# Performance work log

Measured on AMD Instinct MI355X. Metric: run time of the kernel, lower is better.

The kernel has to match this reference:

```python
import jax, jax.numpy as jnp
import numpy as np

N = 50000      # nodes
E = 800000     # edges
D = 128        # input feature dim
H = 8          # heads
U = 32         # units per head (model width = H*U = 256)
L = 2          # attention layers
OUT = 64       # output dim


def setup_inputs() -> dict:
    key = jax.random.key(0)
    ks = jax.random.split(key, 8)
    node_states = jax.random.normal(ks[0], (N, D), jnp.float32)
    edges = jax.random.randint(ks[1], (E, 2), 0, N, jnp.int32)
    s = 0.05  # small init scale keeps pre-clip scores in a sane range
    W_pre = jax.random.normal(ks[2], (D, H * U), jnp.float32) * s
    b_pre = jnp.zeros((H * U,), jnp.float32)
    W_att = jax.random.normal(ks[3], (L, H, H * U, U), jnp.float32) * s
    a_att = jax.random.normal(ks[4], (L, H, 2 * U), jnp.float32) * s
    W_out = jax.random.normal(ks[5], (H * U, OUT), jnp.float32) * s
    b_out = jnp.zeros((OUT,), jnp.float32)
    return {"node_states": node_states, "edges": edges, "W_pre": W_pre,
            "b_pre": b_pre, "W_att": W_att, "a_att": a_att,
            "W_out": W_out, "b_out": b_out}


def _gat_multihead(x, src, dst, W, a):
    """One MultiHeadGraphAttention layer. x:[N,HU], W:[H,HU,U], a:[H,2U].
    Returns relu(concat over heads):[N,HU]."""
    n = x.shape[0]
    h = jnp.einsum('nd,hdu->hnu', x, W)                     # [H,N,U]
    # concat([h_src, h_dst]) @ a  ==  a_src.h_src + a_dst.h_dst
    s_src = jnp.einsum('hnu,hu->hn', h, a[:, :U])           # [H,N]
    s_dst = jnp.einsum('hnu,hu->hn', h, a[:, U:])           # [H,N]
    e = jax.nn.leaky_relu(s_src[:, src] + s_dst[:, dst], negative_slope=0.2)
    e = jnp.exp(jnp.clip(e, -2.0, 2.0))                     # [H,E]
    den = jax.vmap(lambda v: jax.ops.segment_sum(v, src, num_segments=n))(e)
    alpha = e / den[:, src]                                 # [H,E]
    msgs = h[:, dst, :] * alpha[..., None]                  # [H,E,U]
    agg = jax.vmap(lambda m: jax.ops.segment_sum(m, src, num_segments=n))(msgs)
    return jax.nn.relu(agg.transpose(1, 0, 2).reshape(n, -1))  # [N,HU]


def reference(node_states, edges, W_pre, b_pre, W_att, a_att, W_out, b_out):
    src, dst = edges[:, 0], edges[:, 1]
    x = jax.nn.relu(node_states @ W_pre + b_pre)            # [N,HU]
    for l in range(L):
        x = _gat_multihead(x, src, dst, W_att[l], a_att[l]) + x
    return x @ W_out + b_out                                # [N,OUT]
```

## Files before the change

### kernel.cpp

```cpp
#include <hip/hip_runtime.h>
#include <hip/hip_bf16.h>
#include <hip/hip_fp8.h>

#define N_NODES 50000
#define E_EDGES 800000
#define D_IN    128
#define HU      256
#define H_HEADS 8
#define U_DIM   32
#define OUT_DIM 64
#define CAP     64
#define H_SCALE 32.0f

typedef __attribute__((ext_vector_type(8))) short short8v;
typedef __attribute__((ext_vector_type(4))) float f32x4;
typedef unsigned short u16;
typedef unsigned char u8;
typedef __attribute__((ext_vector_type(4))) unsigned short u16x4;
typedef __attribute__((ext_vector_type(8))) unsigned short u16x8;

__device__ __forceinline__ float bf2f(u16 v) {
    return __uint_as_float(((unsigned)v) << 16);
}
__device__ __forceinline__ u16 f2b(float f) {
    unsigned u = __float_as_uint(f);
    return (u16)((u + 0x7FFFu + ((u >> 16) & 1u)) >> 16);
}
__device__ __forceinline__ u8 f2fp8(float f) {
    __hip_fp8_e4m3 t(f);
    return (u8)t.__x;
}

__global__ __launch_bounds__(256) void adj_fill(const int* __restrict__ edges,
                                                int* __restrict__ deg,
                                                u16* __restrict__ adj) {
    int tid = blockIdx.x * 256 + threadIdx.x;
    if (tid >= E_EDGES / 4) return;
    const int4* E4 = (const int4*)edges;
    int4 p0 = E4[tid * 2];
    int4 p1 = E4[tid * 2 + 1];
    int sx[4] = {p0.x, p0.z, p1.x, p1.z};
    int dx[4] = {p0.y, p0.w, p1.y, p1.w};
    int slot[4];
#pragma unroll
    for (int i = 0; i < 4; ++i)
        slot[i] = atomicAdd(&deg[sx[i]], 1);
#pragma unroll
    for (int i = 0; i < 4; ++i)
        if (slot[i] < CAP) adj[(size_t)sx[i] * CAP + slot[i]] = (u16)dx[i];
}

template<int K, int N, bool GAT>
__device__ __forceinline__ void wfrag_one(const float* __restrict__ W,
                                          u16* __restrict__ Wf, int tid) {
    int j  = tid & 7;
    int l  = (tid >> 3) & 63;
    int fb = tid >> 9;
    int ks = fb % (K / 32);
    int ct = fb / (K / 32);
    int k  = ks * 32 + (l >> 4) * 8 + j;
    int n  = ct * 16 + (l & 15);
    float v = GAT ? W[(size_t)(n >> 5) * (K * 32) + k * 32 + (n & 31)]
                  : W[(size_t)k * N + n];
    Wf[tid] = f2b(v);
}

__device__ __forceinline__ void wa_one(const float* __restrict__ Watt,
                                       const float* __restrict__ al,
                                       u16* __restrict__ Wfs, int tid) {
    int j  = tid & 7;
    int l  = (tid >> 3) & 63;
    int ks = tid >> 9;
    int k  = ks * 32 + (l >> 4) * 8 + j;
    int n  = l & 15;
    int hd = n & 7;
    int off = (n < 8) ? 0 : 32;
    float s = 0.f;
#pragma unroll
    for (int u = 0; u < 32; ++u)
        s += Watt[(size_t)hd * 8192 + k * 32 + u] * al[hd * 64 + off + u];
    Wfs[tid] = f2b(s);
}

__global__ __launch_bounds__(256) void wfrag_all(const float* __restrict__ Wpre,
                                                 const float* __restrict__ Watt,
                                                 const float* __restrict__ aatt,
                                                 const float* __restrict__ Wout,
                                                 u16* __restrict__ wf_pre,
                                                 u16* __restrict__ wf_a0,
                                                 u16* __restrict__ wf_a1,
                                                 u16* __restrict__ wf_out,
                                                 u16* __restrict__ wfs0,
                                                 u16* __restrict__ wfs1) {
    int tid = blockIdx.x * 256 + threadIdx.x;
    if (tid < 32768)        wfrag_one<D_IN, HU, false>(Wpre, wf_pre, tid);
    else if (tid < 98304)   wfrag_one<HU, HU, true>(Watt, wf_a0, tid - 32768);
    else if (tid < 163840)  wfrag_one<HU, HU, true>(Watt + 65536, wf_a1, tid - 98304);
    else if (tid < 180224)  wfrag_one<HU, OUT_DIM, false>(Wout, wf_out, tid - 163840);
    else if (tid < 184320)  wa_one(Watt, aatt, wfs0, tid - 180224);
    else if (tid < 188416)  wa_one(Watt + 65536, aatt + 512, wfs1, tid - 184320);
}

template<int K, int N, int MT, int NT, int MODE, bool ABF16>
__global__ __launch_bounds__(256) void mfma_gemm(const void* __restrict__ Ain,
                                                 const u16* __restrict__ Wf,
                                                 const float* __restrict__ bias,
                                                 void* __restrict__ Cout,
                                                 const u16* __restrict__ wfs,
                                                 u16* __restrict__ sb,
                                                 u16* __restrict__ db) {
    constexpr int SK = K + 8;
    __shared__ __align__(16) u16 as[64 * SK];
    int t  = threadIdx.x;
    int n0 = blockIdx.x * 64;

    if (ABF16) {
        constexpr int K8 = K / 8;
        const u16x8* A8 = (const u16x8*)Ain;
        for (int i = t; i < 64 * K8; i += 256) {
            int row = i / K8, c8 = i % K8;
            u16x8 v = {0, 0, 0, 0, 0, 0, 0, 0};
            if (n0 + row < N_NODES)
                v = __builtin_nontemporal_load(&A8[(size_t)(n0 + row) * K8 + c8]);
            *(u16x8*)&as[row * SK + c8 * 8] = v;
        }
    } else {
        constexpr int K4 = K / 4;
        const f32x4* A4 = (const f32x4*)Ain;
        for (int i = t; i < 64 * K4; i += 256) {
            int row = i / K4, c4 = i % K4;
            f32x4 v = {0.f, 0.f, 0.f, 0.f};
            if (n0 + row < N_NODES)
                v = __builtin_nontemporal_load(&A4[(size_t)(n0 + row) * K4 + c4]);
            u16x4 pk;
            pk.x = f2b(v.x); pk.y = f2b(v.y); pk.z = f2b(v.z); pk.w = f2b(v.w);
            *(u16x4*)&as[row * SK + c4 * 4] = pk;
        }
    }
    __syncthreads();

    int wid = t >> 6, l = t & 63;
    constexpr int NWN = N / (NT * 16);
    int col0 = (wid % NWN) * (NT * 16);
    int row0 = (wid / NWN) * (MT * 16);

    f32x4 acc[MT][NT];
#pragma unroll
    for (int mt = 0; mt < MT; ++mt)
#pragma unroll
        for (int nt = 0; nt < NT; ++nt)
            acc[mt][nt] = (f32x4){0.f, 0.f, 0.f, 0.f};
    f32x4 accs[MT];
#pragma unroll
    for (int mt = 0; mt < MT; ++mt) accs[mt] = (f32x4){0.f, 0.f, 0.f, 0.f};

    int ar  = l & 15;
    int akb = (l >> 4) * 8;
#pragma unroll
    for (int ks = 0; ks < K / 32; ++ks) {
        short8v a[MT], b[NT];
#pragma unroll
        for (int mt = 0; mt < MT; ++mt)
            a[mt] = *(const short8v*)&as[(row0 + mt * 16 + ar) * SK + ks * 32 + akb];
#pragma unroll
        for (int nt = 0; nt < NT; ++nt)
            b[nt] = *(const short8v*)&Wf[(size_t)(((((col0 >> 4) + nt) * (K / 32)) + ks) * 64 + l) * 8];
        if (MODE == 1) {
            if (wid == 0) {
                short8v bs = *(const short8v*)&wfs[(size_t)(ks * 64 + l) * 8];
#pragma unroll
                for (int mt = 0; mt < MT; ++mt)
                    accs[mt] = __builtin_amdgcn_mfma_f32_16x16x32_bf16(a[mt], bs, accs[mt], 0, 0, 0);
            }
        }
#pragma unroll
        for (int mt = 0; mt < MT; ++mt)
#pragma unroll
            for (int nt = 0; nt < NT; ++nt)
                acc[mt][nt] = __builtin_amdgcn_mfma_f32_16x16x32_bf16(a[mt], b[nt], acc[mt][nt], 0, 0, 0);
    }

    int crow = (l >> 4) * 4, ccol = l & 15;
#pragma unroll
    for (int mt = 0; mt < MT; ++mt) {
#pragma unroll
        for (int nt = 0; nt < NT; ++nt) {
            int gc = col0 + nt * 16 + ccol;
#pragma unroll
            for (int r = 0; r < 4; ++r) {
                int gr = n0 + row0 + mt * 16 + crow + r;
                if (gr >= N_NODES) continue;
                float v = acc[mt][nt][r];
                if (MODE == 0) {
                    v += bias[gc];
                    ((u16*)Cout)[(size_t)gr * N + gc] = f2b(fmaxf(v, 0.f));
                } else if (MODE == 1) {
                    ((u8*)Cout)[(size_t)gr * N + gc] = f2fp8(v * H_SCALE);
                } else {
                    ((float*)Cout)[(size_t)gr * N + gc] = v + bias[gc];
                }
            }
        }
    }
    if (MODE == 1) {
        if (wid == 0) {
#pragma unroll
            for (int mt = 0; mt < MT; ++mt) {
#pragma unroll
                for (int r = 0; r < 4; ++r) {
                    int gr = n0 + mt * 16 + crow + r;
                    if (gr >= N_NODES) continue;
                    float v = accs[mt][r];
                    if (ccol < 8) sb[(size_t)gr * 8 + ccol] = f2b(v);
                    else          db[(size_t)gr * 8 + ccol - 8] = f2b(v);
                }
            }
        }
    }
}

__global__ __launch_bounds__(256) void agg_kernel(const u8* __restrict__ hb,
                                                  const u16* __restrict__ ssrcb,
                                                  const u16* __restrict__ sdstb,
                                                  const int* __restrict__ deg,
                                                  const u16* __restrict__ adj,
                                                  u16* __restrict__ x) {
    __shared__ u16 sd_lds[4][64 * 8];
    int t  = threadIdx.x & 63;
    int wv = threadIdx.x >> 6;
    int n  = blockIdx.x * 4 + wv;
    int dg = deg[n];
    dg = dg > CAP ? CAP : dg;
    int dl = (t < dg) ? (int)__builtin_nontemporal_load(&adj[(size_t)n * CAP + t]) : 0;
    u16x8 sdrow = *(const u16x8*)(sdstb + (size_t)dl * 8);
    *(u16x8*)&sd_lds[wv][t * 8] = sdrow;
    __syncthreads();

    int hd8 = t & 7;
    float ss_s = bf2f(ssrcb[(size_t)n * 8 + hd8]);
    int q   = t >> 4;
    int sub = t & 15;
    int hdg = sub >> 1;

    float a[16];
#pragma unroll
    for (int i = 0; i < 16; ++i) a[i] = 0.f;
    float den_part = 0.f;

    for (int base = 0; base < dg; base += 8) {
        int eidx = base + (t >> 3);
        float w = 0.f;
        if (eidx < dg) {
            float sc = ss_s + bf2f(sd_lds[wv][eidx * 8 + hd8]);
            sc = sc > 0.f ? sc : 0.2f * sc;
            sc = fminf(fmaxf(sc, -2.f), 2.f);
            w = __expf(sc);
        }
        den_part += w;
#pragma unroll
        for (int g = 0; g < 2; ++g) {
            int e4 = base + g * 4 + q;
            int d  = __shfl(dl, e4);
            float we = __shfl(w, ((g * 4 + q) << 3) | hdg);
            if (e4 < dg) {
                uint4 hv = *(const uint4*)(hb + (size_t)d * HU + sub * 16);
#pragma unroll
                for (int i = 0; i < 4; ++i) {
                    unsigned dw = (&hv.x)[i];
                    auto lo = __builtin_amdgcn_cvt_pk_f32_fp8(dw, false);
                    auto hi = __builtin_amdgcn_cvt_pk_f32_fp8(dw, true);
                    a[4 * i + 0] += we * lo[0];
                    a[4 * i + 1] += we * lo[1];
                    a[4 * i + 2] += we * hi[0];
                    a[4 * i + 3] += we * hi[1];
                }
            }
        }
    }

    den_part += __shfl_xor(den_part, 8);
    den_part += __shfl_xor(den_part, 16);
    den_part += __shfl_xor(den_part, 32);
#pragma unroll
    for (int i = 0; i < 16; ++i) {
        a[i] += __shfl_xor(a[i], 16);
        a[i] += __shfl_xor(a[i], 32);
    }

    if (q == 0) {
        float den = __shfl(den_part, hdg);
        float inv = dg > 0 ? (1.f / den) * (1.f / H_SCALE) : 0.f;
        size_t xo = (size_t)n * HU + sub * 16;
        u16x8 xv0 = __builtin_nontemporal_load((const u16x8*)(x + xo));
        u16x8 xv1 = __builtin_nontemporal_load((const u16x8*)(x + xo + 8));
        u16x8 o0, o1;
#pragma unroll
        for (int i = 0; i < 8; ++i) {
            o0[i] = f2b(fmaxf(a[i] * inv, 0.f) + bf2f((u16)xv0[i]));
            o1[i] = f2b(fmaxf(a[8 + i] * inv, 0.f) + bf2f((u16)xv1[i]));
        }
        __builtin_nontemporal_store(o0, (u16x8*)(x + xo));
        __builtin_nontemporal_store(o1, (u16x8*)(x + xo + 8));
    }
}

extern "C" void kernel_launch(void* const* d_in, const int* in_sizes, int n_in,
                              void* d_out, int out_size, void* d_ws, size_t ws_size,
                              hipStream_t stream) {
    const float* ns   = (const float*)d_in[0];
    const int*   edges= (const int*)d_in[1];
    const float* Wpre = (const float*)d_in[2];
    const float* bpre = (const float*)d_in[3];
    const float* Watt = (const float*)d_in[4];
    const float* aatt = (const float*)d_in[5];
    const float* Wout = (const float*)d_in[6];
    const float* bout = (const float*)d_in[7];
    float* out = (float*)d_out;

    char* p = (char*)d_ws;
    u16* xA = (u16*)p;               p += (size_t)N_NODES * HU * 2;
    u8* h = (u8*)p;                  p += (size_t)N_NODES * HU;
    u16* ssrcb = (u16*)p;            p += (size_t)N_NODES * H_HEADS * 2;
    u16* sdstb = (u16*)p;            p += (size_t)N_NODES * H_HEADS * 2;
    int* deg = (int*)p;              p += (size_t)N_NODES * 4;
    u16* adj = (u16*)p;              p += (size_t)N_NODES * CAP * 2;
    u16* wf_pre  = (u16*)p;          p += (size_t)D_IN * HU * 2;
    u16* wf_att0 = (u16*)p;          p += (size_t)HU * HU * 2;
    u16* wf_att1 = (u16*)p;          p += (size_t)HU * HU * 2;
    u16* wf_out  = (u16*)p;          p += (size_t)HU * OUT_DIM * 2;
    u16* wfs0 = (u16*)p;             p += (size_t)4096 * 2;
    u16* wfs1 = (u16*)p;             p += (size_t)4096 * 2;

    hipMemsetAsync(deg, 0, (size_t)N_NODES * 4, stream);
    adj_fill<<<(E_EDGES / 4 + 255) / 256, 256, 0, stream>>>(edges, deg, adj);

    wfrag_all<<<736, 256, 0, stream>>>(Wpre, Watt, aatt, Wout,
                                       wf_pre, wf_att0, wf_att1, wf_out, wfs0, wfs1);

    const int GB = (N_NODES + 63) / 64;
    mfma_gemm<D_IN, HU, 4, 4, 0, false><<<GB, 256, 0, stream>>>(
        ns, wf_pre, bpre, xA, nullptr, nullptr, nullptr);

    u16* wf_att[2] = {wf_att0, wf_att1};
    u16* wfs[2] = {wfs0, wfs1};
    for (int l = 0; l < 2; ++l) {
        mfma_gemm<HU, HU, 4, 4, 1, true><<<GB, 256, 0, stream>>>(
            xA, wf_att[l], nullptr, h, wfs[l], ssrcb, sdstb);
        agg_kernel<<<(N_NODES / 4), 256, 0, stream>>>(h, ssrcb, sdstb, deg, adj, xA);
    }

    mfma_gemm<HU, OUT_DIM, 1, 4, 2, true><<<GB, 256, 0, stream>>>(
        xA, wf_out, bout, out, nullptr, nullptr, nullptr);
}
```

Before: 242.0 us.

## Fuse adjacency build with pre-GEMM and pad degree counters to avoid contention

```diff
diff --git a/kernel.cpp b/kernel.cpp
--- a/kernel.cpp
+++ b/kernel.cpp
@@ -11,6 +11,7 @@
 #define OUT_DIM 64
 #define CAP     64
 #define H_SCALE 32.0f
+#define DEGS    16
 
 typedef __attribute__((ext_vector_type(8))) short short8v;
 typedef __attribute__((ext_vector_type(4))) float f32x4;
@@ -31,10 +32,8 @@
     return (u8)t.__x;
 }
 
-__global__ __launch_bounds__(256) void adj_fill(const int* __restrict__ edges,
-                                                int* __restrict__ deg,
-                                                u16* __restrict__ adj) {
-    int tid = blockIdx.x * 256 + threadIdx.x;
+__device__ __forceinline__ void adj_body(int tid, const int* __restrict__ edges,
+                                         int* __restrict__ deg, u16* __restrict__ adj) {
     if (tid >= E_EDGES / 4) return;
     const int4* E4 = (const int4*)edges;
     int4 p0 = E4[tid * 2];
@@ -44,7 +43,7 @@
     int slot[4];
 #pragma unroll
     for (int i = 0; i < 4; ++i)
-        slot[i] = atomicAdd(&deg[sx[i]], 1);
+        slot[i] = atomicAdd(&deg[sx[i] * DEGS], 1);
 #pragma unroll
     for (int i = 0; i < 4; ++i)
         if (slot[i] < CAP) adj[(size_t)sx[i] * CAP + slot[i]] = (u16)dx[i];
@@ -91,8 +90,11 @@
                                                  u16* __restrict__ wf_a1,
                                                  u16* __restrict__ wf_out,
                                                  u16* __restrict__ wfs0,
-                                                 u16* __restrict__ wfs1) {
+                                                 u16* __restrict__ wfs1,
+                                                 int* __restrict__ deg) {
     int tid = blockIdx.x * 256 + threadIdx.x;
+    for (int i = tid; i < (N_NODES * DEGS) / 4; i += 736 * 256)
+        ((int4*)deg)[i] = make_int4(0, 0, 0, 0);
     if (tid < 32768)        wfrag_one<D_IN, HU, false>(Wpre, wf_pre, tid);
     else if (tid < 98304)   wfrag_one<HU, HU, true>(Watt, wf_a0, tid - 32768);
     else if (tid < 163840)  wfrag_one<HU, HU, true>(Watt + 65536, wf_a1, tid - 98304);
@@ -102,17 +104,17 @@
 }
 
 template<int K, int N, int MT, int NT, int MODE, bool ABF16>
-__global__ __launch_bounds__(256) void mfma_gemm(const void* __restrict__ Ain,
-                                                 const u16* __restrict__ Wf,
-                                                 const float* __restrict__ bias,
-                                                 void* __restrict__ Cout,
-                                                 const u16* __restrict__ wfs,
-                                                 u16* __restrict__ sb,
-                                                 u16* __restrict__ db) {
+__device__ __forceinline__ void mfma_body(int bid, const void* __restrict__ Ain,
+                                          const u16* __restrict__ Wf,
+                                          const float* __restrict__ bias,
+                                          void* __restrict__ Cout,
+                                          const u16* __restrict__ wfs,
+                                          u16* __restrict__ sb,
+                                          u16* __restrict__ db,
+                                          u16* as) {
     constexpr int SK = K + 8;
-    __shared__ __align__(16) u16 as[64 * SK];
     int t  = threadIdx.x;
-    int n0 = blockIdx.x * 64;
+    int n0 = bid * 64;
 
     if (ABF16) {
         constexpr int K8 = K / 8;
@@ -219,6 +221,37 @@
     }
 }
 
+template<int K, int N, int MT, int NT, int MODE, bool ABF16>
+__global__ __launch_bounds__(256) void mfma_gemm(const void* __restrict__ Ain,
+                                                 const u16* __restrict__ Wf,
+                                                 const float* __restrict__ bias,
+                                                 void* __restrict__ Cout,
+                                                 const u16* __restrict__ wfs,
+                                                 u16* __restrict__ sb,
+                                                 u16* __restrict__ db) {
+    __shared__ __align__(16) u16 as[64 * (K + 8)];
+    mfma_body<K, N, MT, NT, MODE, ABF16>(blockIdx.x, Ain, Wf, bias, Cout, wfs, sb, db, as);
+}
+
+#define ADJ_B 782
+#define GB    782
+__global__ __launch_bounds__(256) void setup_kernel(const int* __restrict__ edges,
+                                                    int* __restrict__ deg,
+                                                    u16* __restrict__ adj,
+                                                    const float* __restrict__ ns,
+                                                    const u16* __restrict__ wf_pre,
+                                                    const float* __restrict__ bpre,
+                                                    u16* __restrict__ xA) {
+    __shared__ __align__(16) u16 as[64 * (D_IN + 8)];
+    int bid = blockIdx.x;
+    if (bid < ADJ_B) {
+        adj_body(bid * 256 + threadIdx.x, edges, deg, adj);
+        return;
+    }
+    mfma_body<D_IN, HU, 4, 4, 0, false>(bid - ADJ_B, ns, wf_pre, bpre, xA,
+                                        nullptr, nullptr, nullptr, as);
+}
+
 __global__ __launch_bounds__(256) void agg_kernel(const u8* __restrict__ hb,
                                                   const u16* __restrict__ ssrcb,
                                                   const u16* __restrict__ sdstb,
@@ -229,7 +262,7 @@
     int t  = threadIdx.x & 63;
     int wv = threadIdx.x >> 6;
     int n  = blockIdx.x * 4 + wv;
-    int dg = deg[n];
+    int dg = deg[(size_t)n * DEGS];
     dg = dg > CAP ? CAP : dg;
     int dl = (t < dg) ? (int)__builtin_nontemporal_load(&adj[(size_t)n * CAP + t]) : 0;
     u16x8 sdrow = *(const u16x8*)(sdstb + (size_t)dl * 8);
@@ -322,7 +355,7 @@
     u8* h = (u8*)p;                  p += (size_t)N_NODES * HU;
     u16* ssrcb = (u16*)p;            p += (size_t)N_NODES * H_HEADS * 2;
     u16* sdstb = (u16*)p;            p += (size_t)N_NODES * H_HEADS * 2;
-    int* deg = (int*)p;              p += (size_t)N_NODES * 4;
+    int* deg = (int*)p;              p += (size_t)N_NODES * DEGS * 4;
     u16* adj = (u16*)p;              p += (size_t)N_NODES * CAP * 2;
     u16* wf_pre  = (u16*)p;          p += (size_t)D_IN * HU * 2;
     u16* wf_att0 = (u16*)p;          p += (size_t)HU * HU * 2;
@@ -331,15 +364,10 @@
     u16* wfs0 = (u16*)p;             p += (size_t)4096 * 2;
     u16* wfs1 = (u16*)p;             p += (size_t)4096 * 2;
 
-    hipMemsetAsync(deg, 0, (size_t)N_NODES * 4, stream);
-    adj_fill<<<(E_EDGES / 4 + 255) / 256, 256, 0, stream>>>(edges, deg, adj);
-
     wfrag_all<<<736, 256, 0, stream>>>(Wpre, Watt, aatt, Wout,
-                                       wf_pre, wf_att0, wf_att1, wf_out, wfs0, wfs1);
-
-    const int GB = (N_NODES + 63) / 64;
-    mfma_gemm<D_IN, HU, 4, 4, 0, false><<<GB, 256, 0, stream>>>(
-        ns, wf_pre, bpre, xA, nullptr, nullptr, nullptr);
+                                       wf_pre, wf_att0, wf_att1, wf_out, wfs0, wfs1, deg);
+
+    setup_kernel<<<ADJ_B + GB, 256, 0, stream>>>(edges, deg, adj, ns, wf_pre, bpre, xA);
 
     u16* wf_att[2] = {wf_att0, wf_att1};
     u16* wfs[2] = {wfs0, wfs1};
```

After: 245.0 us. About the same (+1.2%).

## Pad degree counters, fold memset into weight prep, prefetch gathers for low degree

Applied to the files above, without the earlier changes.

```diff
diff --git a/kernel.cpp b/kernel.cpp
--- a/kernel.cpp
+++ b/kernel.cpp
@@ -11,6 +11,7 @@
 #define OUT_DIM 64
 #define CAP     64
 #define H_SCALE 32.0f
+#define DEGS    16
 
 typedef __attribute__((ext_vector_type(8))) short short8v;
 typedef __attribute__((ext_vector_type(4))) float f32x4;
@@ -44,7 +45,7 @@
     int slot[4];
 #pragma unroll
     for (int i = 0; i < 4; ++i)
-        slot[i] = atomicAdd(&deg[sx[i]], 1);
+        slot[i] = atomicAdd(&deg[sx[i] * DEGS], 1);
 #pragma unroll
     for (int i = 0; i < 4; ++i)
         if (slot[i] < CAP) adj[(size_t)sx[i] * CAP + slot[i]] = (u16)dx[i];
@@ -91,8 +92,11 @@
                                                  u16* __restrict__ wf_a1,
                                                  u16* __restrict__ wf_out,
                                                  u16* __restrict__ wfs0,
-                                                 u16* __restrict__ wfs1) {
+                                                 u16* __restrict__ wfs1,
+                                                 int* __restrict__ deg) {
     int tid = blockIdx.x * 256 + threadIdx.x;
+    for (int i = tid; i < (N_NODES * DEGS) / 4; i += 736 * 256)
+        ((int4*)deg)[i] = make_int4(0, 0, 0, 0);
     if (tid < 32768)        wfrag_one<D_IN, HU, false>(Wpre, wf_pre, tid);
     else if (tid < 98304)   wfrag_one<HU, HU, true>(Watt, wf_a0, tid - 32768);
     else if (tid < 163840)  wfrag_one<HU, HU, true>(Watt + 65536, wf_a1, tid - 98304);
@@ -229,7 +233,7 @@
     int t  = threadIdx.x & 63;
     int wv = threadIdx.x >> 6;
     int n  = blockIdx.x * 4 + wv;
-    int dg = deg[n];
+    int dg = deg[(size_t)n * DEGS];
     dg = dg > CAP ? CAP : dg;
     int dl = (t < dg) ? (int)__builtin_nontemporal_load(&adj[(size_t)n * CAP + t]) : 0;
     u16x8 sdrow = *(const u16x8*)(sdstb + (size_t)dl * 8);
@@ -247,32 +251,82 @@
     for (int i = 0; i < 16; ++i) a[i] = 0.f;
     float den_part = 0.f;
 
-    for (int base = 0; base < dg; base += 8) {
-        int eidx = base + (t >> 3);
-        float w = 0.f;
-        if (eidx < dg) {
-            float sc = ss_s + bf2f(sd_lds[wv][eidx * 8 + hd8]);
-            sc = sc > 0.f ? sc : 0.2f * sc;
-            sc = fminf(fmaxf(sc, -2.f), 2.f);
-            w = __expf(sc);
-        }
-        den_part += w;
-#pragma unroll
-        for (int g = 0; g < 2; ++g) {
-            int e4 = base + g * 4 + q;
-            int d  = __shfl(dl, e4);
-            float we = __shfl(w, ((g * 4 + q) << 3) | hdg);
-            if (e4 < dg) {
-                uint4 hv = *(const uint4*)(hb + (size_t)d * HU + sub * 16);
-#pragma unroll
-                for (int i = 0; i < 4; ++i) {
-                    unsigned dw = (&hv.x)[i];
-                    auto lo = __builtin_amdgcn_cvt_pk_f32_fp8(dw, false);
-                    auto hi = __builtin_amdgcn_cvt_pk_f32_fp8(dw, true);
-                    a[4 * i + 0] += we * lo[0];
-                    a[4 * i + 1] += we * lo[1];
-                    a[4 * i + 2] += we * hi[0];
-                    a[4 * i + 3] += we * hi[1];
+    if (dg <= 32) {
+        int nq = (dg + 3) >> 2;
+        uint4 hv0, hv1, hv2, hv3, hv4, hv5, hv6, hv7;
+        {
+            uint4* hvp[8] = {&hv0, &hv1, &hv2, &hv3, &hv4, &hv5, &hv6, &hv7};
+#pragma unroll
+            for (int i = 0; i < 8; ++i) {
+                if (i < nq) {
+                    int d = __shfl(dl, i * 4 + q);
+                    *hvp[i] = *(const uint4*)(hb + (size_t)d * HU + sub * 16);
+                }
+            }
+        }
+        float w[4];
+#pragma unroll
+        for (int sg = 0; sg < 4; ++sg) {
+            int eidx = sg * 8 + (t >> 3);
+            float ww = 0.f;
+            if (eidx < dg) {
+                float sc = ss_s + bf2f(sd_lds[wv][eidx * 8 + hd8]);
+                sc = sc > 0.f ? sc : 0.2f * sc;
+                sc = fminf(fmaxf(sc, -2.f), 2.f);
+                ww = __expf(sc);
+            }
+            w[sg] = ww;
+            den_part += ww;
+        }
+        const uint4* hvp[8] = {&hv0, &hv1, &hv2, &hv3, &hv4, &hv5, &hv6, &hv7};
+#pragma unroll
+        for (int i = 0; i < 8; ++i) {
+            if (i < nq) {
+                int e4 = i * 4 + q;
+                float we = __shfl(w[i >> 1], ((e4 & 7) << 3) | hdg);
+                if (e4 < dg) {
+                    uint4 hvv = *hvp[i];
+#pragma unroll
+                    for (int k = 0; k < 4; ++k) {
+                        unsigned dw = (&hvv.x)[k];
+                        auto lo = __builtin_amdgcn_cvt_pk_f32_fp8(dw, false);
+                        auto hi = __builtin_amdgcn_cvt_pk_f32_fp8(dw, true);
+                        a[4 * k + 0] += we * lo[0];
+                        a[4 * k + 1] += we * lo[1];
+                        a[4 * k + 2] += we * hi[0];
+                        a[4 * k + 3] += we * hi[1];
+                    }
+                }
+            }
+        }
+    } else {
+        for (int base = 0; base < dg; base += 8) {
+            int eidx = base + (t >> 3);
+            float w = 0.f;
+            if (eidx < dg) {
+                float sc = ss_s + bf2f(sd_lds[wv][eidx * 8 + hd8]);
+                sc = sc > 0.f ? sc : 0.2f * sc;
+                sc = fminf(fmaxf(sc, -2.f), 2.f);
+                w = __expf(sc);
+            }
+            den_part += w;
+#pragma unroll
+            for (int g = 0; g < 2; ++g) {
+                int e4 = base + g * 4 + q;
+                int d  = __shfl(dl, e4);
+                float we = __shfl(w, ((g * 4 + q) << 3) | hdg);
+                if (e4 < dg) {
+                    uint4 hvv = *(const uint4*)(hb + (size_t)d * HU + sub * 16);
+#pragma unroll
+                    for (int k = 0; k < 4; ++k) {
+                        unsigned dw = (&hvv.x)[k];
+                        auto lo = __builtin_amdgcn_cvt_pk_f32_fp8(dw, false);
+                        auto hi = __builtin_amdgcn_cvt_pk_f32_fp8(dw, true);
+                        a[4 * k + 0] += we * lo[0];
+                        a[4 * k + 1] += we * lo[1];
+                        a[4 * k + 2] += we * hi[0];
+                        a[4 * k + 3] += we * hi[1];
+                    }
                 }
             }
         }
@@ -322,7 +376,7 @@
     u8* h = (u8*)p;                  p += (size_t)N_NODES * HU;
     u16* ssrcb = (u16*)p;            p += (size_t)N_NODES * H_HEADS * 2;
     u16* sdstb = (u16*)p;            p += (size_t)N_NODES * H_HEADS * 2;
-    int* deg = (int*)p;              p += (size_t)N_NODES * 4;
+    int* deg = (int*)p;              p += (size_t)N_NODES * DEGS * 4;
     u16* adj = (u16*)p;              p += (size_t)N_NODES * CAP * 2;
     u16* wf_pre  = (u16*)p;          p += (size_t)D_IN * HU * 2;
     u16* wf_att0 = (u16*)p;          p += (size_t)HU * HU * 2;
@@ -331,11 +385,10 @@
     u16* wfs0 = (u16*)p;             p += (size_t)4096 * 2;
     u16* wfs1 = (u16*)p;             p += (size_t)4096 * 2;
 
-    hipMemsetAsync(deg, 0, (size_t)N_NODES * 4, stream);
+    wfrag_all<<<736, 256, 0, stream>>>(Wpre, Watt, aatt, Wout,
+                                       wf_pre, wf_att0, wf_att1, wf_out, wfs0, wfs1, deg);
+
     adj_fill<<<(E_EDGES / 4 + 255) / 256, 256, 0, stream>>>(edges, deg, adj);
-
-    wfrag_all<<<736, 256, 0, stream>>>(Wpre, Watt, aatt, Wout,
-                                       wf_pre, wf_att0, wf_att1, wf_out, wfs0, wfs1);
 
     const int GB = (N_NODES + 63) / 64;
     mfma_gemm<D_IN, HU, 4, 4, 0, false><<<GB, 256, 0, stream>>>(
```

After: 239.4 us. Within noise of the previous version (-1.1%).
